# Kernel optimization log

Measured on AMD Instinct MI355X. Metric: run time of the kernel, lower is better.

The kernel has to match this reference:

```python
import jax, jax.numpy as jnp
import numpy as np

B, IN, OUT, E, H, K = 8192, 1024, 256, 16, 512, 3
EPS = 1e-10


def setup_inputs() -> dict:
    key = jax.random.key(0)
    ks = jax.random.split(key, 5)
    scaled = lambda k, shape, fan: jax.random.normal(k, shape, jnp.float32) / np.sqrt(fan)
    return {
        "x": jax.random.normal(ks[0], (B, IN), jnp.float32),
        # torch init is zeros for w_gate (degenerate ties); use small random for a meaningful reference
        "w_gate": jax.random.normal(ks[1], (IN, E), jnp.float32) * 0.02,
        "W1": scaled(ks[2], (E, IN, H), IN),
        "b1": jnp.zeros((E, H), jnp.float32),
        "W2": scaled(ks[3], (E, H, OUT), H),
        "b2": jnp.zeros((E, OUT), jnp.float32),
    }


def _cv_squared(v):
    # torch .var() is unbiased (ddof=1)
    return jnp.var(v, ddof=1) / (jnp.mean(v) ** 2 + EPS)


def reference(x, w_gate, W1, b1, W2, b2):
    # --- top-k gating (eval mode: clean logits, no noise) ---
    logits = x @ w_gate                                   # [B, E]
    top_vals, top_idx = jax.lax.top_k(logits, K)          # [B, K]
    top_gates = jax.nn.softmax(top_vals, axis=-1)         # softmax over selected k
    rows = jnp.arange(logits.shape[0])[:, None]
    gates = jnp.zeros_like(logits).at[rows, top_idx].set(top_gates)  # sparse gates [B, E]

    # --- load-balancing loss ---
    importance = gates.sum(0)
    load = (gates > 0).sum(0).astype(jnp.float32)         # _gates_to_load (eval path)
    loss = _cv_squared(importance) + _cv_squared(load)

    # --- experts (MLP stand-in; dense compute, sparse combine via zero gates) ---
    h = jax.nn.relu(jnp.einsum('bi,eih->beh', x, W1) + b1)  # [B, E, H]
    expert_out = jnp.einsum('beh,eho->beo', h, W2) + b2     # [B, E, OUT]

    # combine: equivalent to SparseDispatcher gather/split/scatter-add with gate weighting
    y = jnp.einsum('be,beo->bo', gates, expert_out)         # [B, OUT]
    return y, loss
```

## Files before the change

### kernel.cpp

```cpp
#include <hip/hip_runtime.h>

#define B_ 8192
#define IN_ 1024
#define OUT_ 256
#define E_ 16
#define KTOP 3
#define H_ 512
#define MAXSLOTS 26624
#define NTILES 208
#define HBLK 16

typedef __bf16 bf16;
typedef __bf16 bf16x4 __attribute__((ext_vector_type(4)));
typedef __bf16 bf16x8 __attribute__((ext_vector_type(8)));
typedef float f32x4 __attribute__((ext_vector_type(4)));

__device__ __forceinline__ void async16(const bf16* g, bf16* l) {
    __builtin_amdgcn_global_load_lds(
        (const __attribute__((address_space(1))) void*)g,
        (__attribute__((address_space(3))) void*)l,
        16, 0, 0);
}

__global__ __launch_bounds__(256) void k_init(
    int* __restrict__ row_ids, int* __restrict__ tile_expert,
    bf16* __restrict__ zero_row,
    const float* __restrict__ wg, float* __restrict__ wgT) {
    int id = blockIdx.x * 256 + threadIdx.x;
    if (id < MAXSLOTS) row_ids[id] = -1;
    if (id < NTILES) tile_expert[id] = -1;
    if (id < IN_) zero_row[id] = (bf16)0.f;
    if (id < E_ * IN_) {
        int e = id >> 10, j = id & 1023;
        wgT[id] = wg[j * E_ + e];
    }
}

__global__ __launch_bounds__(256) void k_transpose(
    const float* __restrict__ W1, bf16* __restrict__ w1t,
    const float* __restrict__ W2, bf16* __restrict__ w2t) {
    __shared__ float tile[64][65];
    int bx = blockIdx.x;
    const float* in; bf16* out; int Kd, Nd, e, tk, tn;
    if (bx < 2048) {
        in = W1; out = w1t; Kd = IN_; Nd = H_;
        e = bx >> 7; int tt = bx & 127; tk = tt >> 3; tn = tt & 7;
    } else {
        bx -= 2048;
        in = W2; out = w2t; Kd = H_; Nd = OUT_;
        e = bx >> 5; int tt = bx & 31; tk = tt >> 2; tn = tt & 3;
    }
    int t = threadIdx.x;
    int r = t >> 6, c = t & 63;
    const float* src = in + ((size_t)e * Kd + tk * 64) * Nd + (size_t)tn * 64;
#pragma unroll
    for (int i = 0; i < 16; i++) {
        int rr = r + i * 4;
        tile[rr][c] = src[(size_t)rr * Nd + c];
    }
    __syncthreads();
    bf16* dst = out + ((size_t)e * Nd + tn * 64) * Kd + (size_t)tk * 64;
#pragma unroll
    for (int i = 0; i < 16; i++) {
        int rr = r + i * 4;
        dst[(size_t)rr * Kd + c] = (bf16)tile[c][rr];
    }
}

__global__ __launch_bounds__(256) void k_gating(
    const float* __restrict__ x, const float* __restrict__ wgT,
    bf16* __restrict__ xbf, int* __restrict__ top_idx, float* __restrict__ top_gate) {
    int t = threadIdx.x;
    int row = blockIdx.x * 4 + (t >> 6);
    int lane = t & 63;
    float acc[16];
#pragma unroll
    for (int e = 0; e < 16; e++) acc[e] = 0.f;
    const float4* x4p = (const float4*)(x + (size_t)row * IN_);
    const float4* w4 = (const float4*)wgT;
#pragma unroll
    for (int it = 0; it < 4; it++) {
        int j0 = it * 64 + lane;
        float4 xv = x4p[j0];
        bf16x4 xb;
        xb[0] = (bf16)xv.x; xb[1] = (bf16)xv.y; xb[2] = (bf16)xv.z; xb[3] = (bf16)xv.w;
        *(bf16x4*)(xbf + (size_t)row * IN_ + j0 * 4) = xb;
#pragma unroll
        for (int e = 0; e < 16; e++) {
            float4 wv = w4[e * 256 + j0];
            acc[e] += xv.x * wv.x + xv.y * wv.y + xv.z * wv.z + xv.w * wv.w;
        }
    }
#pragma unroll
    for (int e = 0; e < 16; e++) {
#pragma unroll
        for (int s = 32; s > 0; s >>= 1) acc[e] += __shfl_xor(acc[e], s, 64);
    }
    if (lane == 0) {
        float v[16];
#pragma unroll
        for (int e = 0; e < 16; e++) v[e] = acc[e];
        int idx[KTOP];
        float val[KTOP];
#pragma unroll
        for (int k = 0; k < KTOP; k++) {
            int best = 0;
            float bv = v[0];
            for (int e = 1; e < 16; e++) {
                if (v[e] > bv) { bv = v[e]; best = e; }
            }
            idx[k] = best; val[k] = bv; v[best] = -1e30f;
        }
        float e1 = __expf(val[1] - val[0]);
        float e2 = __expf(val[2] - val[0]);
        float inv = 1.f / (1.f + e1 + e2);
        float g[KTOP] = {inv, e1 * inv, e2 * inv};
#pragma unroll
        for (int k = 0; k < KTOP; k++) {
            top_idx[row * KTOP + k] = idx[k];
            top_gate[row * KTOP + k] = g[k];
        }
    }
}

__global__ __launch_bounds__(256) void k_hist(
    const int* __restrict__ top_idx, int* __restrict__ partial) {
    __shared__ int wcnt[4][16];
    int t = threadIdx.x;
    int w = t >> 6, lane = t & 63;
    int blk = blockIdx.x;
    int cnt[16];
#pragma unroll
    for (int k = 0; k < 16; k++) cnt[k] = 0;
#pragma unroll
    for (int j = 0; j < 6; j++) {
        int e = top_idx[blk * 1536 + j * 256 + t];
#pragma unroll
        for (int k = 0; k < 16; k++)
            cnt[k] += (int)__popcll(__ballot(e == k));
    }
    if (lane == 0) {
#pragma unroll
        for (int k = 0; k < 16; k++) wcnt[w][k] = cnt[k];
    }
    __syncthreads();
    if (t < 16) partial[blk * 16 + t] = wcnt[0][t] + wcnt[1][t] + wcnt[2][t] + wcnt[3][t];
}

__global__ __launch_bounds__(256) void k_scan(
    const int* __restrict__ partial, int* __restrict__ counts,
    int* __restrict__ tile_expert, int* __restrict__ gbase) {
    __shared__ int sp[HBLK * 16];
    __shared__ int soff[16];
    int t = threadIdx.x;
    sp[t] = partial[t];
    __syncthreads();
    if (t < 16) {
        int s = 0;
#pragma unroll
        for (int b = 0; b < HBLK; b++) s += sp[b * 16 + t];
        counts[t] = s;
    }
    __syncthreads();
    if (t == 0) {
        int off = 0;
        for (int e = 0; e < E_; e++) {
            int c = 0;
#pragma unroll
            for (int b = 0; b < HBLK; b++) c += sp[b * 16 + e];
            soff[e] = off;
            int pd = (c + 127) & ~127;
            int t0 = off >> 7, t1 = (off + pd) >> 7;
            for (int tt = t0; tt < t1; ++tt) tile_expert[tt] = e;
            off += pd;
        }
    }
    __syncthreads();
    {
        int b = t >> 4, e = t & 15;
        int s = soff[e];
        for (int bp = 0; bp < b; bp++) s += sp[bp * 16 + e];
        gbase[t] = s;
    }
}

__global__ __launch_bounds__(256) void k_scatter(
    const int* __restrict__ top_idx, const float* __restrict__ top_gate,
    const int* __restrict__ gbase,
    int* __restrict__ row_ids, int* __restrict__ rowslot,
    float* __restrict__ partial_imp) {
    __shared__ int lcnt[16];
    __shared__ float limp[16];
    int t = threadIdx.x;
    int blk = blockIdx.x;
    if (t < 16) { lcnt[t] = 0; limp[t] = 0.f; }
    __syncthreads();
#pragma unroll
    for (int j = 0; j < 6; j++) {
        int gid = blk * 1536 + j * 256 + t;
        int e = top_idx[gid];
        float g = top_gate[gid];
        int rank = atomicAdd(&lcnt[e], 1);
        atomicAdd(&limp[e], g);
        int slot = gbase[blk * 16 + e] + rank;
        row_ids[slot] = gid / KTOP;
        rowslot[gid] = slot;
    }
    __syncthreads();
    if (t < 16) partial_imp[blk * 16 + t] = limp[t];
}


__global__ __launch_bounds__(256) void k_gemm1(
    const bf16* __restrict__ xbf, const bf16* __restrict__ w1t,
    const float* __restrict__ b1, const int* __restrict__ row_ids,
    const int* __restrict__ tile_expert, const bf16* __restrict__ zero_row,
    bf16* __restrict__ h) {
    int e = tile_expert[blockIdx.y];
    if (e < 0) return;
    int slot_base = blockIdx.y * 128;
    int nbase = blockIdx.x * 128;
    __shared__ __align__(16) bf16 As[128 * 64];
    __shared__ __align__(16) bf16 Bs[128 * 64];
    int t = threadIdx.x;
    int rmod = (t >> 3) & 7;
    int cglob = (t & 7) ^ rmod;
    const bf16* gA[4];
    const bf16* gB[4];
#pragma unroll
    for (int j = 0; j < 4; j++) {
        int m = j * 32 + (t >> 3);
        int rid = row_ids[slot_base + m];
        gA[j] = ((rid >= 0) ? xbf + (size_t)rid * IN_ : zero_row) + cglob * 8;
        gB[j] = w1t + ((size_t)e * H_ + nbase + m) * IN_ + cglob * 8;
    }
    int w = t >> 6, lane = t & 63;
    int wm = (w >> 1) * 64, wn = (w & 1) * 64;
    int lm = lane & 15, lq = lane >> 4;
    f32x4 acc[4][4] = {};
    for (int k0 = 0; k0 < IN_; k0 += 64) {
#pragma unroll
        for (int j = 0; j < 4; j++) {
            async16(gA[j] + k0, As + (j * 256 + t) * 8);
            async16(gB[j] + k0, Bs + (j * 256 + t) * 8);
        }
        __syncthreads();
        const bf16x8* Av = (const bf16x8*)As;
        const bf16x8* Bv = (const bf16x8*)Bs;
#pragma unroll
        for (int ks = 0; ks < 2; ks++) {
            int kc = ks * 4 + lq;
            bf16x8 af[4], bfv[4];
#pragma unroll
            for (int i = 0; i < 4; i++) {
                int row = wm + i * 16 + lm;
                af[i] = Av[row * 8 + (kc ^ (row & 7))];
            }
#pragma unroll
            for (int i = 0; i < 4; i++) {
                int row = wn + i * 16 + lm;
                bfv[i] = Bv[row * 8 + (kc ^ (row & 7))];
            }
#pragma unroll
            for (int mi = 0; mi < 4; mi++)
#pragma unroll
                for (int ni = 0; ni < 4; ni++)
                    acc[mi][ni] = __builtin_amdgcn_mfma_f32_16x16x32_bf16(af[mi], bfv[ni], acc[mi][ni], 0, 0, 0);
        }
        __syncthreads();
    }
#pragma unroll
    for (int mi = 0; mi < 4; mi++) {
#pragma unroll
        for (int ni = 0; ni < 4; ni++) {
            int colg = nbase + wn + ni * 16 + lm;
            float bias = b1[e * H_ + colg];
#pragma unroll
            for (int r = 0; r < 4; r++) {
                int rowl = wm + mi * 16 + lq * 4 + r;
                float v = acc[mi][ni][r] + bias;
                v = v > 0.f ? v : 0.f;
                h[(size_t)(slot_base + rowl) * H_ + colg] = (bf16)v;
            }
        }
    }
}

__global__ __launch_bounds__(256) void k_gemm2(
    const bf16* __restrict__ h, const bf16* __restrict__ w2t,
    const float* __restrict__ b2, const int* __restrict__ tile_expert,
    float* __restrict__ eout) {
    int e = tile_expert[blockIdx.y];
    if (e < 0) return;
    int slot_base = blockIdx.y * 128;
    int nbase = blockIdx.x * 128;
    __shared__ __align__(16) bf16 As[128 * 64];
    __shared__ __align__(16) bf16 Bs[128 * 64];
    int t = threadIdx.x;
    int rmod = (t >> 3) & 7;
    int cglob = (t & 7) ^ rmod;
    const bf16* gA[4];
    const bf16* gB[4];
#pragma unroll
    for (int j = 0; j < 4; j++) {
        int m = j * 32 + (t >> 3);
        gA[j] = h + (size_t)(slot_base + m) * H_ + cglob * 8;
        gB[j] = w2t + ((size_t)e * OUT_ + nbase + m) * H_ + cglob * 8;
    }
    int w = t >> 6, lane = t & 63;
    int wm = (w >> 1) * 64, wn = (w & 1) * 64;
    int lm = lane & 15, lq = lane >> 4;
    f32x4 acc[4][4] = {};
    for (int k0 = 0; k0 < H_; k0 += 64) {
#pragma unroll
        for (int j = 0; j < 4; j++) {
            async16(gA[j] + k0, As + (j * 256 + t) * 8);
            async16(gB[j] + k0, Bs + (j * 256 + t) * 8);
        }
        __syncthreads();
        const bf16x8* Av = (const bf16x8*)As;
        const bf16x8* Bv = (const bf16x8*)Bs;
#pragma unroll
        for (int ks = 0; ks < 2; ks++) {
            int kc = ks * 4 + lq;
            bf16x8 af[4], bfv[4];
#pragma unroll
            for (int i = 0; i < 4; i++) {
                int row = wm + i * 16 + lm;
                af[i] = Av[row * 8 + (kc ^ (row & 7))];
            }
#pragma unroll
            for (int i = 0; i < 4; i++) {
                int row = wn + i * 16 + lm;
                bfv[i] = Bv[row * 8 + (kc ^ (row & 7))];
            }
#pragma unroll
            for (int mi = 0; mi < 4; mi++)
#pragma unroll
                for (int ni = 0; ni < 4; ni++)
                    acc[mi][ni] = __builtin_amdgcn_mfma_f32_16x16x32_bf16(af[mi], bfv[ni], acc[mi][ni], 0, 0, 0);
        }
        __syncthreads();
    }
#pragma unroll
    for (int mi = 0; mi < 4; mi++) {
#pragma unroll
        for (int ni = 0; ni < 4; ni++) {
            int colg = nbase + wn + ni * 16 + lm;
            float bias = b2[e * OUT_ + colg];
#pragma unroll
            for (int r = 0; r < 4; r++) {
                int rowl = wm + mi * 16 + lq * 4 + r;
                eout[(size_t)(slot_base + rowl) * OUT_ + colg] = acc[mi][ni][r] + bias;
            }
        }
    }
}

__global__ __launch_bounds__(256) void k_combine(
    const float* __restrict__ eout, const int* __restrict__ rowslot,
    const float* __restrict__ top_gate, float* __restrict__ y) {
    int t = threadIdx.x;
    int b = blockIdx.x * 4 + (t >> 6);
    int lane = t & 63;
    int s0 = rowslot[b * 3], s1 = rowslot[b * 3 + 1], s2 = rowslot[b * 3 + 2];
    float g0 = top_gate[b * 3], g1 = top_gate[b * 3 + 1], g2 = top_gate[b * 3 + 2];
    const float4* e4 = (const float4*)eout;
    float4 v0 = e4[(size_t)s0 * 64 + lane];
    float4 v1 = e4[(size_t)s1 * 64 + lane];
    float4 v2 = e4[(size_t)s2 * 64 + lane];
    float4 r;
    r.x = g0 * v0.x + g1 * v1.x + g2 * v2.x;
    r.y = g0 * v0.y + g1 * v1.y + g2 * v2.y;
    r.z = g0 * v0.z + g1 * v1.z + g2 * v2.z;
    r.w = g0 * v0.w + g1 * v1.w + g2 * v2.w;
    ((float4*)y)[(size_t)b * 64 + lane] = r;
}

__global__ void k_loss(const float* __restrict__ partial_imp, const int* __restrict__ counts,
                       float* __restrict__ loss_out) {
    __shared__ float imp[16];
    int t = threadIdx.x;
    if (t < 16) {
        float s = 0.f;
#pragma unroll
        for (int b = 0; b < HBLK; b++) s += partial_imp[b * 16 + t];
        imp[t] = s;
    }
    __syncthreads();
    if (t == 0) {
        float si = 0.f, sl = 0.f;
        for (int e = 0; e < E_; e++) { si += imp[e]; sl += (float)counts[e]; }
        float mi_ = si / (float)E_, ml_ = sl / (float)E_;
        float vi = 0.f, vl = 0.f;
        for (int e = 0; e < E_; e++) {
            float d = imp[e] - mi_; vi += d * d;
            float d2 = (float)counts[e] - ml_; vl += d2 * d2;
        }
        vi /= (float)(E_ - 1); vl /= (float)(E_ - 1);
        *loss_out = vi / (mi_ * mi_ + 1e-10f) + vl / (ml_ * ml_ + 1e-10f);
    }
}

extern "C" void kernel_launch(void* const* d_in, const int* in_sizes, int n_in,
                              void* d_out, int out_size, void* d_ws, size_t ws_size,
                              hipStream_t stream) {
    (void)in_sizes; (void)n_in; (void)out_size; (void)ws_size;
    const float* x = (const float*)d_in[0];
    const float* wgate = (const float*)d_in[1];
    const float* W1 = (const float*)d_in[2];
    const float* b1 = (const float*)d_in[3];
    const float* W2 = (const float*)d_in[4];
    const float* b2 = (const float*)d_in[5];
    float* y = (float*)d_out;

    char* p = (char*)d_ws;
    auto alloc = [&](size_t bytes) {
        char* q = p;
        p += (bytes + 255) & ~(size_t)255;
        return q;
    };
    bf16* xbf = (bf16*)alloc((size_t)B_ * IN_ * 2);
    bf16* w1t = (bf16*)alloc((size_t)E_ * H_ * IN_ * 2);
    bf16* w2t = (bf16*)alloc((size_t)E_ * OUT_ * H_ * 2);
    bf16* h = (bf16*)alloc((size_t)MAXSLOTS * H_ * 2);
    int* row_ids = (int*)alloc((size_t)MAXSLOTS * 4);
    int* rowslot = (int*)alloc((size_t)B_ * KTOP * 4);
    int* top_idx = (int*)alloc((size_t)B_ * KTOP * 4);
    float* top_gate = (float*)alloc((size_t)B_ * KTOP * 4);
    int* counts = (int*)alloc(E_ * 4);
    int* partial = (int*)alloc(HBLK * E_ * 4);
    int* gbase = (int*)alloc(HBLK * E_ * 4);
    float* partial_imp = (float*)alloc(HBLK * E_ * 4);
    int* tile_expert = (int*)alloc(NTILES * 4);
    bf16* zero_row = (bf16*)alloc(IN_ * 2);
    float* wgT = (float*)alloc((size_t)E_ * IN_ * 4);
    float* eout = (float*)xbf;

    k_init<<<dim3((MAXSLOTS + 255) / 256), dim3(256), 0, stream>>>(
        row_ids, tile_expert, zero_row, wgate, wgT);
    k_transpose<<<dim3(2048 + 512), dim3(256), 0, stream>>>(W1, w1t, W2, w2t);
    k_gating<<<dim3(B_ / 4), dim3(256), 0, stream>>>(x, wgT, xbf, top_idx, top_gate);
    k_hist<<<dim3(HBLK), dim3(256), 0, stream>>>(top_idx, partial);
    k_scan<<<dim3(1), dim3(256), 0, stream>>>(partial, counts, tile_expert, gbase);
    k_scatter<<<dim3(HBLK), dim3(256), 0, stream>>>(
        top_idx, top_gate, gbase, row_ids, rowslot, partial_imp);
    k_gemm1<<<dim3(H_ / 128, NTILES), dim3(256), 0, stream>>>(
        xbf, w1t, b1, row_ids, tile_expert, zero_row, h);
    k_gemm2<<<dim3(OUT_ / 128, NTILES), dim3(256), 0, stream>>>(
        h, w2t, b2, tile_expert, eout);
    k_combine<<<dim3(B_ / 4), dim3(256), 0, stream>>>(eout, rowslot, top_gate, y);
    k_loss<<<dim3(1), dim3(64), 0, stream>>>(partial_imp, counts, y + (size_t)B_ * OUT_);
}
```

Measured before the change: 221.3 us.

## Fuse setup, dispatch and loss kernels to cut launch count; swap GEMM grid axes

```diff
diff --git a/kernel.cpp b/kernel.cpp
--- a/kernel.cpp
+++ b/kernel.cpp
@@ -22,35 +22,38 @@
         16, 0, 0);
 }
 
-__global__ __launch_bounds__(256) void k_init(
-    int* __restrict__ row_ids, int* __restrict__ tile_expert,
-    bf16* __restrict__ zero_row,
-    const float* __restrict__ wg, float* __restrict__ wgT) {
-    int id = blockIdx.x * 256 + threadIdx.x;
-    if (id < MAXSLOTS) row_ids[id] = -1;
-    if (id < NTILES) tile_expert[id] = -1;
-    if (id < IN_) zero_row[id] = (bf16)0.f;
-    if (id < E_ * IN_) {
-        int e = id >> 10, j = id & 1023;
-        wgT[id] = wg[j * E_ + e];
-    }
-}
-
-__global__ __launch_bounds__(256) void k_transpose(
+__global__ __launch_bounds__(256) void k_setup(
     const float* __restrict__ W1, bf16* __restrict__ w1t,
-    const float* __restrict__ W2, bf16* __restrict__ w2t) {
+    const float* __restrict__ W2, bf16* __restrict__ w2t,
+    int* __restrict__ row_ids, const float* __restrict__ wg, float* __restrict__ wgT,
+    bf16* __restrict__ zero_row, int* __restrict__ tile_expert) {
+    int bx = blockIdx.x;
+    int t = threadIdx.x;
+    if (bx >= 2560) {
+        if (bx < 2664) {
+            int id = (bx - 2560) * 256 + t;
+            if (id < MAXSLOTS) row_ids[id] = -1;
+        } else if (bx < 2728) {
+            int id = (bx - 2664) * 256 + t;
+            int e = id >> 10, j = id & 1023;
+            wgT[id] = wg[j * E_ + e];
+        } else {
+#pragma unroll
+            for (int i = 0; i < 4; i++) zero_row[t * 4 + i] = (bf16)0.f;
+            if (t < NTILES) tile_expert[t] = -1;
+        }
+        return;
+    }
     __shared__ float tile[64][65];
-    int bx = blockIdx.x;
     const float* in; bf16* out; int Kd, Nd, e, tk, tn;
     if (bx < 2048) {
         in = W1; out = w1t; Kd = IN_; Nd = H_;
         e = bx >> 7; int tt = bx & 127; tk = tt >> 3; tn = tt & 7;
     } else {
-        bx -= 2048;
+        int b2x = bx - 2048;
         in = W2; out = w2t; Kd = H_; Nd = OUT_;
-        e = bx >> 5; int tt = bx & 31; tk = tt >> 2; tn = tt & 3;
-    }
-    int t = threadIdx.x;
+        e = b2x >> 5; int tt = b2x & 31; tk = tt >> 2; tn = tt & 3;
+    }
     int r = t >> 6, c = t & 63;
     const float* src = in + ((size_t)e * Kd + tk * 64) * Nd + (size_t)tn * 64;
 #pragma unroll
@@ -123,77 +126,57 @@
     }
 }
 
-__global__ __launch_bounds__(256) void k_hist(
-    const int* __restrict__ top_idx, int* __restrict__ partial) {
-    __shared__ int wcnt[4][16];
-    int t = threadIdx.x;
-    int w = t >> 6, lane = t & 63;
+__global__ __launch_bounds__(256) void k_dispatch(
+    const int* __restrict__ top_idx, const float* __restrict__ top_gate,
+    int* __restrict__ counts, int* __restrict__ tile_expert,
+    int* __restrict__ row_ids, int* __restrict__ rowslot,
+    float* __restrict__ partial_imp) {
+    __shared__ int wtot[4][16];
+    __shared__ int wpre[4][16];
+    __shared__ int sbase[16];
+    __shared__ int lcnt[16];
+    __shared__ float limp[16];
+    int t = threadIdx.x;
+    int w = t >> 6;
     int blk = blockIdx.x;
-    int cnt[16];
-#pragma unroll
-    for (int k = 0; k < 16; k++) cnt[k] = 0;
-#pragma unroll
-    for (int j = 0; j < 6; j++) {
-        int e = top_idx[blk * 1536 + j * 256 + t];
-#pragma unroll
-        for (int k = 0; k < 16; k++)
-            cnt[k] += (int)__popcll(__ballot(e == k));
-    }
+    int tot[16], pre[16];
+#pragma unroll
+    for (int k = 0; k < 16; k++) { tot[k] = 0; pre[k] = 0; }
+    for (int c = 0; c < HBLK; c++) {
+#pragma unroll
+        for (int j = 0; j < 6; j++) {
+            int e = top_idx[c * 1536 + j * 256 + t];
+#pragma unroll
+            for (int k = 0; k < 16; k++) {
+                int n = (int)__popcll(__ballot(e == k));
+                tot[k] += n;
+                if (c < blk) pre[k] += n;
+            }
+        }
+    }
+    int lane = t & 63;
     if (lane == 0) {
 #pragma unroll
-        for (int k = 0; k < 16; k++) wcnt[w][k] = cnt[k];
-    }
-    __syncthreads();
-    if (t < 16) partial[blk * 16 + t] = wcnt[0][t] + wcnt[1][t] + wcnt[2][t] + wcnt[3][t];
-}
-
-__global__ __launch_bounds__(256) void k_scan(
-    const int* __restrict__ partial, int* __restrict__ counts,
-    int* __restrict__ tile_expert, int* __restrict__ gbase) {
-    __shared__ int sp[HBLK * 16];
-    __shared__ int soff[16];
-    int t = threadIdx.x;
-    sp[t] = partial[t];
+        for (int k = 0; k < 16; k++) { wtot[w][k] = tot[k]; wpre[w][k] = pre[k]; }
+    }
+    if (t < 16) { lcnt[t] = 0; limp[t] = 0.f; }
     __syncthreads();
     if (t < 16) {
-        int s = 0;
-#pragma unroll
-        for (int b = 0; b < HBLK; b++) s += sp[b * 16 + t];
-        counts[t] = s;
-    }
-    __syncthreads();
-    if (t == 0) {
         int off = 0;
-        for (int e = 0; e < E_; e++) {
-            int c = 0;
-#pragma unroll
-            for (int b = 0; b < HBLK; b++) c += sp[b * 16 + e];
-            soff[e] = off;
-            int pd = (c + 127) & ~127;
-            int t0 = off >> 7, t1 = (off + pd) >> 7;
-            for (int tt = t0; tt < t1; ++tt) tile_expert[tt] = e;
-            off += pd;
-        }
-    }
-    __syncthreads();
-    {
-        int b = t >> 4, e = t & 15;
-        int s = soff[e];
-        for (int bp = 0; bp < b; bp++) s += sp[bp * 16 + e];
-        gbase[t] = s;
-    }
-}
-
-__global__ __launch_bounds__(256) void k_scatter(
-    const int* __restrict__ top_idx, const float* __restrict__ top_gate,
-    const int* __restrict__ gbase,
-    int* __restrict__ row_ids, int* __restrict__ rowslot,
-    float* __restrict__ partial_imp) {
-    __shared__ int lcnt[16];
-    __shared__ float limp[16];
-    int t = threadIdx.x;
-    int blk = blockIdx.x;
-    if (t < 16) { lcnt[t] = 0; limp[t] = 0.f; }
+        for (int e = 0; e < 16; e++) {
+            int ce = wtot[0][e] + wtot[1][e] + wtot[2][e] + wtot[3][e];
+            if (e == t) break;
+            off += (ce + 127) & ~127;
+        }
+        int cnt_t = wtot[0][t] + wtot[1][t] + wtot[2][t] + wtot[3][t];
+        int pre_t = wpre[0][t] + wpre[1][t] + wpre[2][t] + wpre[3][t];
+        sbase[t] = off + pre_t;
+        if (blk == 0) {
+            counts[t] = cnt_t;
+            int pd = (cnt_t + 127) & ~127;
+            for (int tt = off >> 7; tt < (off + pd) >> 7; ++tt) tile_expert[tt] = t;
+        }
+    }
     __syncthreads();
 #pragma unroll
     for (int j = 0; j < 6; j++) {
@@ -202,7 +185,7 @@
         float g = top_gate[gid];
         int rank = atomicAdd(&lcnt[e], 1);
         atomicAdd(&limp[e], g);
-        int slot = gbase[blk * 16 + e] + rank;
+        int slot = sbase[e] + rank;
         row_ids[slot] = gid / KTOP;
         rowslot[gid] = slot;
     }
@@ -216,10 +199,10 @@
     const float* __restrict__ b1, const int* __restrict__ row_ids,
     const int* __restrict__ tile_expert, const bf16* __restrict__ zero_row,
     bf16* __restrict__ h) {
-    int e = tile_expert[blockIdx.y];
+    int e = tile_expert[blockIdx.x];
     if (e < 0) return;
-    int slot_base = blockIdx.y * 128;
-    int nbase = blockIdx.x * 128;
+    int slot_base = blockIdx.x * 128;
+    int nbase = blockIdx.y * 128;
     __shared__ __align__(16) bf16 As[128 * 64];
     __shared__ __align__(16) bf16 Bs[128 * 64];
     int t = threadIdx.x;
@@ -290,10 +273,10 @@
     const bf16* __restrict__ h, const bf16* __restrict__ w2t,
     const float* __restrict__ b2, const int* __restrict__ tile_expert,
     float* __restrict__ eout) {
-    int e = tile_expert[blockIdx.y];
+    int e = tile_expert[blockIdx.x];
     if (e < 0) return;
-    int slot_base = blockIdx.y * 128;
-    int nbase = blockIdx.x * 128;
+    int slot_base = blockIdx.x * 128;
+    int nbase = blockIdx.y * 128;
     __shared__ __align__(16) bf16 As[128 * 64];
     __shared__ __align__(16) bf16 Bs[128 * 64];
     int t = threadIdx.x;
@@ -359,8 +342,33 @@
 
 __global__ __launch_bounds__(256) void k_combine(
     const float* __restrict__ eout, const int* __restrict__ rowslot,
-    const float* __restrict__ top_gate, float* __restrict__ y) {
-    int t = threadIdx.x;
+    const float* __restrict__ top_gate, float* __restrict__ y,
+    const float* __restrict__ partial_imp, const int* __restrict__ counts,
+    float* __restrict__ loss_out) {
+    int t = threadIdx.x;
+    if (blockIdx.x == B_ / 4) {
+        __shared__ float imp[16];
+        if (t < 16) {
+            float s = 0.f;
+#pragma unroll
+            for (int b = 0; b < HBLK; b++) s += partial_imp[b * 16 + t];
+            imp[t] = s;
+        }
+        __syncthreads();
+        if (t == 0) {
+            float si = 0.f, sl = 0.f;
+            for (int e = 0; e < E_; e++) { si += imp[e]; sl += (float)counts[e]; }
+            float mi_ = si / (float)E_, ml_ = sl / (float)E_;
+            float vi = 0.f, vl = 0.f;
+            for (int e = 0; e < E_; e++) {
+                float d = imp[e] - mi_; vi += d * d;
+                float d2 = (float)counts[e] - ml_; vl += d2 * d2;
+            }
+            vi /= (float)(E_ - 1); vl /= (float)(E_ - 1);
+            *loss_out = vi / (mi_ * mi_ + 1e-10f) + vl / (ml_ * ml_ + 1e-10f);
+        }
+        return;
+    }
     int b = blockIdx.x * 4 + (t >> 6);
     int lane = t & 63;
     int s0 = rowslot[b * 3], s1 = rowslot[b * 3 + 1], s2 = rowslot[b * 3 + 2];
@@ -375,31 +383,6 @@
     r.z = g0 * v0.z + g1 * v1.z + g2 * v2.z;
     r.w = g0 * v0.w + g1 * v1.w + g2 * v2.w;
     ((float4*)y)[(size_t)b * 64 + lane] = r;
-}
-
-__global__ void k_loss(const float* __restrict__ partial_imp, const int* __restrict__ counts,
-                       float* __restrict__ loss_out) {
-    __shared__ float imp[16];
-    int t = threadIdx.x;
-    if (t < 16) {
-        float s = 0.f;
-#pragma unroll
-        for (int b = 0; b < HBLK; b++) s += partial_imp[b * 16 + t];
-        imp[t] = s;
-    }
-    __syncthreads();
-    if (t == 0) {
-        float si = 0.f, sl = 0.f;
-        for (int e = 0; e < E_; e++) { si += imp[e]; sl += (float)counts[e]; }
-        float mi_ = si / (float)E_, ml_ = sl / (float)E_;
-        float vi = 0.f, vl = 0.f;
-        for (int e = 0; e < E_; e++) {
-            float d = imp[e] - mi_; vi += d * d;
-            float d2 = (float)counts[e] - ml_; vl += d2 * d2;
-        }
-        vi /= (float)(E_ - 1); vl /= (float)(E_ - 1);
-        *loss_out = vi / (mi_ * mi_ + 1e-10f) + vl / (ml_ * ml_ + 1e-10f);
-    }
 }
 
 extern "C" void kernel_launch(void* const* d_in, const int* in_sizes, int n_in,
@@ -429,26 +412,21 @@
     int* top_idx = (int*)alloc((size_t)B_ * KTOP * 4);
     float* top_gate = (float*)alloc((size_t)B_ * KTOP * 4);
     int* counts = (int*)alloc(E_ * 4);
-    int* partial = (int*)alloc(HBLK * E_ * 4);
-    int* gbase = (int*)alloc(HBLK * E_ * 4);
     float* partial_imp = (float*)alloc(HBLK * E_ * 4);
     int* tile_expert = (int*)alloc(NTILES * 4);
     bf16* zero_row = (bf16*)alloc(IN_ * 2);
     float* wgT = (float*)alloc((size_t)E_ * IN_ * 4);
     float* eout = (float*)xbf;
 
-    k_init<<<dim3((MAXSLOTS + 255) / 256), dim3(256), 0, stream>>>(
-        row_ids, tile_expert, zero_row, wgate, wgT);
-    k_transpose<<<dim3(2048 + 512), dim3(256), 0, stream>>>(W1, w1t, W2, w2t);
+    k_setup<<<dim3(2729), dim3(256), 0, stream>>>(
+        W1, w1t, W2, w2t, row_ids, wgate, wgT, zero_row, tile_expert);
     k_gating<<<dim3(B_ / 4), dim3(256), 0, stream>>>(x, wgT, xbf, top_idx, top_gate);
-    k_hist<<<dim3(HBLK), dim3(256), 0, stream>>>(top_idx, partial);
-    k_scan<<<dim3(1), dim3(256), 0, stream>>>(partial, counts, tile_expert, gbase);
-    k_scatter<<<dim3(HBLK), dim3(256), 0, stream>>>(
-        top_idx, top_gate, gbase, row_ids, rowslot, partial_imp);
-    k_gemm1<<<dim3(H_ / 128, NTILES), dim3(256), 0, stream>>>(
+    k_dispatch<<<dim3(HBLK), dim3(256), 0, stream>>>(
+        top_idx, top_gate, counts, tile_expert, row_ids, rowslot, partial_imp);
+    k_gemm1<<<dim3(NTILES, H_ / 128), dim3(256), 0, stream>>>(
         xbf, w1t, b1, row_ids, tile_expert, zero_row, h);
-    k_gemm2<<<dim3(OUT_ / 128, NTILES), dim3(256), 0, stream>>>(
+    k_gemm2<<<dim3(NTILES, OUT_ / 128), dim3(256), 0, stream>>>(
         h, w2t, b2, tile_expert, eout);
-    k_combine<<<dim3(B_ / 4), dim3(256), 0, stream>>>(eout, rowslot, top_gate, y);
-    k_loss<<<dim3(1), dim3(64), 0, stream>>>(partial_imp, counts, y + (size_t)B_ * OUT_);
-}
+    k_combine<<<dim3(B_ / 4 + 1), dim3(256), 0, stream>>>(
+        eout, rowslot, top_gate, y, partial_imp, counts, y + (size_t)B_ * OUT_);
+}
```

Result: slower. 244.3 us (+10.4%).
